# Optimization experiments

Hardware: AMD Instinct MI355X
Metric: run time of the kernel (lower is better)

## Reference

```python
import jax, jax.numpy as jnp
import numpy as np

EMBED_DIM = 768
NUM_HEADS = 12
HEAD_SIZE = EMBED_DIM // NUM_HEADS


def setup_inputs() -> dict:
    key = jax.random.key(0)
    ks = jax.random.split(key, 9)
    B, S, D = 4, 2048, EMBED_DIM
    scale = 1.0 / np.sqrt(D)
    x = jax.random.normal(ks[0], (B, S, D), dtype=jnp.float32)
    # Linear params (torch nn.Linear: y = x @ W.T + b); store W as [in, out] for einsum
    Wq = jax.random.normal(ks[1], (D, D), dtype=jnp.float32) * scale
    bq = jnp.zeros((D,), dtype=jnp.float32)
    Wk = jax.random.normal(ks[2], (D, D), dtype=jnp.float32) * scale
    bk = jnp.zeros((D,), dtype=jnp.float32)
    Wv = jax.random.normal(ks[3], (D, D), dtype=jnp.float32) * scale
    bv = jnp.zeros((D,), dtype=jnp.float32)
    Wo = jax.random.normal(ks[4], (D, D), dtype=jnp.float32) * scale
    bo = jnp.zeros((D,), dtype=jnp.float32)
    return {"x": x, "Wq": Wq, "bq": bq, "Wk": Wk, "bk": bk,
            "Wv": Wv, "bv": bv, "Wo": Wo, "bo": bo}


def reference(x, Wq, bq, Wk, bk, Wv, bv, Wo, bo):
    B, S, D = x.shape
    H, hs = NUM_HEADS, HEAD_SIZE
    scale = hs ** (-0.5)
    # Projections
    Q = (x @ Wq + bq).reshape(B, S, H, hs)
    K = (x @ Wk + bk).reshape(B, S, H, hs)
    V = (x @ Wv + bv).reshape(B, S, H, hs)
    # Batched attention over all heads (equivalent to the per-head loop:
    # torch view splits last dim into H contiguous chunks; concat of per-head
    # outputs along -1 restores the same layout)
    scores = jnp.einsum('bqhd,bkhd->bhqk', Q, K) * scale  # [B,H,S,S]
    attn = jax.nn.softmax(scores, axis=-1)
    out = jnp.einsum('bhqk,bkhd->bqhd', attn, V).reshape(B, S, D)
    # Output projection; dropout is identity in eval mode
    return out @ Wo + bo
```

## Files before the change

### kernel.cpp

```cpp
#include <hip/hip_runtime.h>

typedef unsigned short ushort_t;
typedef __bf16 bf16x8 __attribute__((ext_vector_type(8)));
typedef float floatx4 __attribute__((ext_vector_type(4)));

__device__ inline ushort_t f2bf(float f) {
    __bf16 h = (__bf16)f;
    return __builtin_bit_cast(ushort_t, h);
}

__device__ inline void gload16(const void* g, void* l) {
    __builtin_amdgcn_global_load_lds((const __attribute__((address_space(1))) void*)g,
                                     (__attribute__((address_space(3))) void*)l, 16, 0, 0);
}

__global__ __launch_bounds__(256) void prep_kernel(
    const float* __restrict__ x, ushort_t* __restrict__ xbf,
    const float* __restrict__ W0, const float* __restrict__ W1,
    const float* __restrict__ W2, const float* __restrict__ W3,
    ushort_t* __restrict__ T0, ushort_t* __restrict__ T1,
    ushort_t* __restrict__ T2, ushort_t* __restrict__ T3) {
    int bx = blockIdx.x;
    int tid = threadIdx.x;
    if (bx < 2304) {
        __shared__ float t[32][33];
        int w = bx / 576, rem = bx % 576;
        const float* W; ushort_t* T;
        switch (w) {
            case 0: W = W0; T = T0; break;
            case 1: W = W1; T = T1; break;
            case 2: W = W2; T = T2; break;
            default: W = W3; T = T3; break;
        }
        int n0 = (rem / 24) * 32, k0 = (rem % 24) * 32;
        int tx = tid & 31, ty = tid >> 5;
        for (int i = 0; i < 4; ++i)
            t[ty + i * 8][tx] = W[(k0 + ty + i * 8) * 768 + n0 + tx];
        __syncthreads();
        for (int i = 0; i < 4; ++i)
            T[(n0 + ty + i * 8) * 768 + k0 + tx] = f2bf(t[tx][ty + i * 8]);
    } else {
        int i = ((bx - 2304) * 256 + tid) * 4;
        float4 v = *(const float4*)(x + i);
        ushort4 u;
        u.x = f2bf(v.x); u.y = f2bf(v.y); u.z = f2bf(v.z); u.w = f2bf(v.w);
        *(ushort4*)(xbf + i) = u;
    }
}

__global__ __launch_bounds__(256) void gemm_qkv(
    const ushort_t* __restrict__ A,
    const ushort_t* __restrict__ Tq, const ushort_t* __restrict__ Tk, const ushort_t* __restrict__ Tv,
    const float* __restrict__ bq, const float* __restrict__ bk, const float* __restrict__ bv,
    ushort_t* __restrict__ Qb, ushort_t* __restrict__ Kb, ushort_t* __restrict__ Vtb) {
    __shared__ ushort_t sh[128 * 64 + 64 * 64];
    ushort_t* As = sh;
    ushort_t* Bs = sh + 128 * 64;
    int tid = threadIdx.x;
    int m0 = blockIdx.x * 128;
    int by = blockIdx.y;
    int which = by / 12;
    int n0 = (by % 12) * 64;
    const ushort_t* Bt = which == 0 ? Tq : (which == 1 ? Tk : Tv);
    const float* bias = which == 0 ? bq : (which == 1 ? bk : bv);

    int wave = tid >> 6;
    int lane = tid & 63;
    int ln = tid & 15;
    int quad = (tid >> 4) & 3;
    int wm = wave * 32;
    int lr = lane >> 3;
    int lc = (lane & 7) * 8;

    floatx4 acc[2][4];
    floatx4 z = {0.f, 0.f, 0.f, 0.f};
    for (int i = 0; i < 2; ++i)
        for (int j = 0; j < 4; ++j) acc[i][j] = z;

    for (int kt = 0; kt < 12; ++kt) {
        int k0 = kt * 64;
        __syncthreads();
        for (int i = 0; i < 4; ++i) {
            int c = wave * 4 + i;
            gload16(&A[(m0 + c * 8 + lr) * 768 + k0 + lc], &As[c * 512]);
        }
        for (int i = 0; i < 2; ++i) {
            int c = wave * 2 + i;
            gload16(&Bt[(n0 + c * 8 + lr) * 768 + k0 + lc], &Bs[c * 512]);
        }
        __syncthreads();
        for (int ks = 0; ks < 2; ++ks) {
            bf16x8 a[2], b[4];
            for (int i = 0; i < 2; ++i)
                a[i] = *(const bf16x8*)&As[(wm + i * 16 + ln) * 64 + ks * 32 + quad * 8];
            for (int j = 0; j < 4; ++j)
                b[j] = *(const bf16x8*)&Bs[(j * 16 + ln) * 64 + ks * 32 + quad * 8];
            for (int i = 0; i < 2; ++i)
                for (int j = 0; j < 4; ++j)
                    acc[i][j] = __builtin_amdgcn_mfma_f32_16x16x32_bf16(a[i], b[j], acc[i][j], 0, 0, 0);
        }
    }

    const float QSCALE = 0.125f * 1.44269504088896f;
    if (which != 2) {
        for (int i = 0; i < 2; ++i) {
            for (int j = 0; j < 4; ++j) {
                int gn = n0 + j * 16 + ln;
                float bia = bias[gn];
                int h = gn >> 6, dd = gn & 63;
                for (int r = 0; r < 4; ++r) {
                    int gm = m0 + wm + i * 16 + quad * 4 + r;
                    int bb = gm >> 11, ss = gm & 2047;
                    float v = acc[i][j][r] + bia;
                    if (which == 0) {
                        Qb[((bb * 12 + h) * 2048 + ss) * 64 + dd] = f2bf(v * QSCALE);
                    } else {
                        Kb[((bb * 12 + h) * 2048 + ss) * 64 + dd] = f2bf(v);
                    }
                }
            }
        }
    } else {
        __syncthreads();
        ushort_t* tr = sh;
        for (int j = 0; j < 4; ++j) {
            int nl = j * 16 + ln;
            float bia = bias[n0 + nl];
            for (int i = 0; i < 2; ++i) {
                ushort4 u;
                u.x = f2bf(acc[i][j][0] + bia);
                u.y = f2bf(acc[i][j][1] + bia);
                u.z = f2bf(acc[i][j][2] + bia);
                u.w = f2bf(acc[i][j][3] + bia);
                *(ushort4*)&tr[nl * 136 + wm + i * 16 + quad * 4] = u;
            }
        }
        __syncthreads();
        int bb = m0 >> 11, ss0 = m0 & 2047;
        int head = by % 12;
        for (int p = 0; p < 4; ++p) {
            int n = p * 16 + (tid >> 4);
            int mc = (tid & 15) * 8;
            uint4 v = *(const uint4*)&tr[n * 136 + mc];
            *(uint4*)&Vtb[(size_t)((bb * 12 + head) * 64 + n) * 2048 + ss0 + mc] = v;
        }
    }
}

__global__ __launch_bounds__(256, 2) void attn_kernel(
    const ushort_t* __restrict__ Qb, const ushort_t* __restrict__ Kb,
    const ushort_t* __restrict__ Vtb, ushort_t* __restrict__ Ob) {
    __shared__ ushort_t shm[4 * 64 * 72];
    const int PANEL = 64 * 72;
    int tid = threadIdx.x;
    int bid = blockIdx.x;
    int swz = (bid & 7) * 96 + (bid >> 3);
    int bh = swz >> 4;
    int qt = swz & 15;
    int wave = tid >> 6;
    int qh = wave >> 1;
    int kh = wave & 1;
    int ln = tid & 15;
    int quad = (tid >> 4) & 3;
    int q0 = qt * 128 + qh * 64;

    const ushort_t* Qp = Qb + (size_t)bh * 2048 * 64;
    const ushort_t* Kp = Kb + (size_t)bh * 2048 * 64;
    const ushort_t* Vp = Vtb + (size_t)bh * 64 * 2048;

    bf16x8 bqf[4][2];
    for (int g = 0; g < 4; ++g)
        for (int ks = 0; ks < 2; ++ks)
            bqf[g][ks] = *(const bf16x8*)&Qp[(q0 + g * 16 + ln) * 64 + ks * 32 + quad * 8];

    int srow = tid >> 3;
    int c8 = tid & 7;
    int scol = c8 * 8;
    int u = c8 & 3;
    int vcol = (c8 >> 2) * 32 + (u & 1) * 16 + (u >> 1) * 4;

    uint4 kreg[2], vreg[2];

    for (int p = 0; p < 2; ++p) {
        kreg[p] = *(const uint4*)&Kp[(p * 32 + srow) * 64 + scol];
        vreg[p] = *(const uint4*)&Vp[(p * 32 + srow) * 2048 + scol];
    }
    for (int p = 0; p < 2; ++p) {
        *(uint4*)&shm[(p * 32 + srow) * 72 + scol] = kreg[p];
        ushort_t* vb = &shm[2 * PANEL + (p * 32 + srow) * 72 + vcol];
        *(uint2*)vb = make_uint2(vreg[p].x, vreg[p].y);
        *(uint2*)(vb + 8) = make_uint2(vreg[p].z, vreg[p].w);
    }
    __syncthreads();

    floatx4 o_acc[4][4];
    float lsum[4] = {0.f, 0.f, 0.f, 0.f};
    floatx4 z = {0.f, 0.f, 0.f, 0.f};
    for (int g = 0; g < 4; ++g)
        for (int m4 = 0; m4 < 4; ++m4) o_acc[g][m4] = z;

    for (int kt = 0; kt < 32; ++kt) {
        int cur = kt & 1;
        if (kt < 31) {
            for (int p = 0; p < 2; ++p) {
                kreg[p] = *(const uint4*)&Kp[((kt + 1) * 64 + p * 32 + srow) * 64 + scol];
                vreg[p] = *(const uint4*)&Vp[(p * 32 + srow) * 2048 + (kt + 1) * 64 + scol];
            }
        }

        const ushort_t* KsH = shm + cur * PANEL;
        const ushort_t* VsH = shm + (2 + cur) * PANEL;

        bf16x8 ak[2][2];
        for (int m = 0; m < 2; ++m)
            for (int ks = 0; ks < 2; ++ks)
                ak[m][ks] = *(const bf16x8*)&KsH[((kh * 2 + m) * 16 + ln) * 72 + ks * 32 + quad * 8];

        floatx4 st[4][2];
        for (int g = 0; g < 4; ++g)
            for (int m = 0; m < 2; ++m) {
                floatx4 s = z;
                s = __builtin_amdgcn_mfma_f32_16x16x32_bf16(ak[m][0], bqf[g][0], s, 0, 0, 0);
                s = __builtin_amdgcn_mfma_f32_16x16x32_bf16(ak[m][1], bqf[g][1], s, 0, 0, 0);
                st[g][m] = s;
            }

        for (int g = 0; g < 4; ++g)
            for (int m = 0; m < 2; ++m)
                for (int r = 0; r < 4; ++r) {
                    float e = __builtin_amdgcn_exp2f(st[g][m][r]);
                    st[g][m][r] = e;
                    lsum[g] += e;
                }

        bf16x8 av[4];
        for (int m4 = 0; m4 < 4; ++m4)
            av[m4] = *(const bf16x8*)&VsH[(m4 * 16 + ln) * 72 + kh * 32 + quad * 8];

        for (int g = 0; g < 4; ++g) {
            bf16x8 b;
            b[0] = (__bf16)st[g][0][0];
            b[1] = (__bf16)st[g][0][1];
            b[2] = (__bf16)st[g][0][2];
            b[3] = (__bf16)st[g][0][3];
            b[4] = (__bf16)st[g][1][0];
            b[5] = (__bf16)st[g][1][1];
            b[6] = (__bf16)st[g][1][2];
            b[7] = (__bf16)st[g][1][3];
            for (int m4 = 0; m4 < 4; ++m4)
                o_acc[g][m4] = __builtin_amdgcn_mfma_f32_16x16x32_bf16(av[m4], b, o_acc[g][m4], 0, 0, 0);
        }

        if (kt < 31) {
            int nxt = cur ^ 1;
            ushort_t* Kn = shm + nxt * PANEL;
            ushort_t* Vn = shm + (2 + nxt) * PANEL;
            for (int p = 0; p < 2; ++p) {
                *(uint4*)&Kn[(p * 32 + srow) * 72 + scol] = kreg[p];
                ushort_t* vb = &Vn[(p * 32 + srow) * 72 + vcol];
                *(uint2*)vb = make_uint2(vreg[p].x, vreg[p].y);
                *(uint2*)(vb + 8) = make_uint2(vreg[p].z, vreg[p].w);
            }
        }
        __syncthreads();
    }

    for (int g = 0; g < 4; ++g) {
        lsum[g] += __shfl_xor(lsum[g], 16);
        lsum[g] += __shfl_xor(lsum[g], 32);
    }

    float* mbuf = (float*)shm;
    float* lbuf = mbuf + 2 * 64 * 68;
    if (kh == 1) {
        float* base = mbuf + qh * 64 * 68;
        for (int g = 0; g < 4; ++g) {
            for (int m4 = 0; m4 < 4; ++m4)
                *(floatx4*)&base[(g * 16 + ln) * 68 + m4 * 16 + quad * 4] = o_acc[g][m4];
            if (quad == 0) lbuf[qh * 64 + g * 16 + ln] = lsum[g];
        }
    }
    __syncthreads();

    int b = bh / 12, h = bh % 12;
    if (kh == 0) {
        float* base = mbuf + qh * 64 * 68;
        for (int g = 0; g < 4; ++g) {
            float inv = 1.f / (lsum[g] + lbuf[qh * 64 + g * 16 + ln]);
            int token = b * 2048 + q0 + g * 16 + ln;
            for (int m4 = 0; m4 < 4; ++m4) {
                floatx4 o2 = *(const floatx4*)&base[(g * 16 + ln) * 68 + m4 * 16 + quad * 4];
                for (int r = 0; r < 4; ++r)
                    Ob[token * 768 + h * 64 + m4 * 16 + quad * 4 + r] =
                        f2bf((o_acc[g][m4][r] + o2[r]) * inv);
            }
        }
    }
}

__global__ __launch_bounds__(256) void gemm_out(
    const ushort_t* __restrict__ A, const ushort_t* __restrict__ Bt,
    const float* __restrict__ bias, float* __restrict__ out) {
    __shared__ ushort_t As[128 * 64];
    __shared__ ushort_t Bs[64 * 64];
    int tid = threadIdx.x;
    int m0 = blockIdx.x * 128;
    int n0 = blockIdx.y * 64;

    int wave = tid >> 6;
    int lane = tid & 63;
    int ln = tid & 15;
    int quad = (tid >> 4) & 3;
    int wm = wave * 32;
    int lr = lane >> 3;
    int lc = (lane & 7) * 8;

    floatx4 acc[2][4];
    floatx4 z = {0.f, 0.f, 0.f, 0.f};
    for (int i = 0; i < 2; ++i)
        for (int j = 0; j < 4; ++j) acc[i][j] = z;

    for (int kt = 0; kt < 12; ++kt) {
        int k0 = kt * 64;
        __syncthreads();
        for (int i = 0; i < 4; ++i) {
            int c = wave * 4 + i;
            gload16(&A[(m0 + c * 8 + lr) * 768 + k0 + lc], &As[c * 512]);
        }
        for (int i = 0; i < 2; ++i) {
            int c = wave * 2 + i;
            gload16(&Bt[(n0 + c * 8 + lr) * 768 + k0 + lc], &Bs[c * 512]);
        }
        __syncthreads();
        for (int ks = 0; ks < 2; ++ks) {
            bf16x8 a[2], b[4];
            for (int i = 0; i < 2; ++i)
                a[i] = *(const bf16x8*)&As[(wm + i * 16 + ln) * 64 + ks * 32 + quad * 8];
            for (int j = 0; j < 4; ++j)
                b[j] = *(const bf16x8*)&Bs[(j * 16 + ln) * 64 + ks * 32 + quad * 8];
            for (int i = 0; i < 2; ++i)
                for (int j = 0; j < 4; ++j)
                    acc[i][j] = __builtin_amdgcn_mfma_f32_16x16x32_bf16(a[i], b[j], acc[i][j], 0, 0, 0);
        }
    }

    for (int i = 0; i < 2; ++i) {
        for (int j = 0; j < 4; ++j) {
            int gn = n0 + j * 16 + ln;
            float bia = bias[gn];
            for (int r = 0; r < 4; ++r) {
                int gm = m0 + wm + i * 16 + quad * 4 + r;
                out[gm * 768 + gn] = acc[i][j][r] + bia;
            }
        }
    }
}

extern "C" void kernel_launch(void* const* d_in, const int* in_sizes, int n_in,
                              void* d_out, int out_size, void* d_ws, size_t ws_size,
                              hipStream_t stream) {
    const float* x  = (const float*)d_in[0];
    const float* Wq = (const float*)d_in[1];
    const float* bq = (const float*)d_in[2];
    const float* Wk = (const float*)d_in[3];
    const float* bk = (const float*)d_in[4];
    const float* Wv = (const float*)d_in[5];
    const float* bv = (const float*)d_in[6];
    const float* Wo = (const float*)d_in[7];
    const float* bo = (const float*)d_in[8];

    const int NTOK = 4 * 2048;
    const int NELT = NTOK * 768;
    const int WELT = 768 * 768;

    ushort_t* xbf = (ushort_t*)d_ws;
    ushort_t* Tq  = xbf + NELT;
    ushort_t* Tk  = Tq + WELT;
    ushort_t* Tv  = Tk + WELT;
    ushort_t* To  = Tv + WELT;
    ushort_t* Qb  = To + WELT;
    ushort_t* Kb  = Qb + NELT;
    ushort_t* Vtb = Kb + NELT;
    ushort_t* Ob  = Vtb + NELT;

    prep_kernel<<<8448, 256, 0, stream>>>(x, xbf, Wq, Wk, Wv, Wo, Tq, Tk, Tv, To);
    gemm_qkv<<<dim3(64, 36), 256, 0, stream>>>(xbf, Tq, Tk, Tv, bq, bk, bv, Qb, Kb, Vtb);
    attn_kernel<<<768, 256, 0, stream>>>(Qb, Kb, Vtb, Ob);
    gemm_out<<<dim3(64, 12), 256, 0, stream>>>(Ob, To, bo, (float*)d_out);
}
```

Baseline: 214.4 us.

## Fuse Q, K, V projections into one block sharing the A tile

```diff
diff --git a/kernel.cpp b/kernel.cpp
--- a/kernel.cpp
+++ b/kernel.cpp
@@ -48,21 +48,16 @@
     }
 }
 
-__global__ __launch_bounds__(256) void gemm_qkv(
+__global__ __launch_bounds__(256, 2) void gemm_qkv(
     const ushort_t* __restrict__ A,
     const ushort_t* __restrict__ Tq, const ushort_t* __restrict__ Tk, const ushort_t* __restrict__ Tv,
     const float* __restrict__ bq, const float* __restrict__ bk, const float* __restrict__ bv,
     ushort_t* __restrict__ Qb, ushort_t* __restrict__ Kb, ushort_t* __restrict__ Vtb) {
-    __shared__ ushort_t sh[128 * 64 + 64 * 64];
-    ushort_t* As = sh;
-    ushort_t* Bs = sh + 128 * 64;
+    __shared__ ushort_t sh[128 * 64 + 3 * 64 * 64];
     int tid = threadIdx.x;
     int m0 = blockIdx.x * 128;
     int by = blockIdx.y;
-    int which = by / 12;
-    int n0 = (by % 12) * 64;
-    const ushort_t* Bt = which == 0 ? Tq : (which == 1 ? Tk : Tv);
-    const float* bias = which == 0 ? bq : (which == 1 ? bk : bv);
+    int n0 = by * 64;
 
     int wave = tid >> 6;
     int lane = tid & 63;
@@ -72,37 +67,48 @@
     int lr = lane >> 3;
     int lc = (lane & 7) * 8;
 
-    floatx4 acc[2][4];
+    floatx4 acc[3][2][4];
     floatx4 z = {0.f, 0.f, 0.f, 0.f};
-    for (int i = 0; i < 2; ++i)
-        for (int j = 0; j < 4; ++j) acc[i][j] = z;
+    for (int w = 0; w < 3; ++w)
+        for (int i = 0; i < 2; ++i)
+            for (int j = 0; j < 4; ++j) acc[w][i][j] = z;
 
     for (int kt = 0; kt < 12; ++kt) {
         int k0 = kt * 64;
         __syncthreads();
         for (int i = 0; i < 4; ++i) {
             int c = wave * 4 + i;
-            gload16(&A[(m0 + c * 8 + lr) * 768 + k0 + lc], &As[c * 512]);
+            gload16(&A[(m0 + c * 8 + lr) * 768 + k0 + lc], &sh[c * 512]);
         }
         for (int i = 0; i < 2; ++i) {
             int c = wave * 2 + i;
-            gload16(&Bt[(n0 + c * 8 + lr) * 768 + k0 + lc], &Bs[c * 512]);
+            int goff = (n0 + c * 8 + lr) * 768 + k0 + lc;
+            gload16(&Tq[goff], &sh[8192 + c * 512]);
+            gload16(&Tk[goff], &sh[12288 + c * 512]);
+            gload16(&Tv[goff], &sh[16384 + c * 512]);
         }
         __syncthreads();
         for (int ks = 0; ks < 2; ++ks) {
-            bf16x8 a[2], b[4];
+            bf16x8 a[2];
             for (int i = 0; i < 2; ++i)
-                a[i] = *(const bf16x8*)&As[(wm + i * 16 + ln) * 64 + ks * 32 + quad * 8];
-            for (int j = 0; j < 4; ++j)
-                b[j] = *(const bf16x8*)&Bs[(j * 16 + ln) * 64 + ks * 32 + quad * 8];
-            for (int i = 0; i < 2; ++i)
+                a[i] = *(const bf16x8*)&sh[(wm + i * 16 + ln) * 64 + ks * 32 + quad * 8];
+            for (int w = 0; w < 3; ++w) {
+                const ushort_t* Bs = &sh[8192 + w * 4096];
+                bf16x8 b[4];
                 for (int j = 0; j < 4; ++j)
-                    acc[i][j] = __builtin_amdgcn_mfma_f32_16x16x32_bf16(a[i], b[j], acc[i][j], 0, 0, 0);
+                    b[j] = *(const bf16x8*)&Bs[(j * 16 + ln) * 64 + ks * 32 + quad * 8];
+                for (int i = 0; i < 2; ++i)
+                    for (int j = 0; j < 4; ++j)
+                        acc[w][i][j] = __builtin_amdgcn_mfma_f32_16x16x32_bf16(a[i], b[j], acc[w][i][j], 0, 0, 0);
+            }
         }
     }
 
     const float QSCALE = 0.125f * 1.44269504088896f;
-    if (which != 2) {
+    for (int w = 0; w < 2; ++w) {
+        const float* bias = w == 0 ? bq : bk;
+        ushort_t* QK = w == 0 ? Qb : Kb;
+        float scale = w == 0 ? QSCALE : 1.0f;
         for (int i = 0; i < 2; ++i) {
             for (int j = 0; j < 4; ++j) {
                 int gn = n0 + j * 16 + ln;
@@ -111,33 +117,29 @@
                 for (int r = 0; r < 4; ++r) {
                     int gm = m0 + wm + i * 16 + quad * 4 + r;
                     int bb = gm >> 11, ss = gm & 2047;
-                    float v = acc[i][j][r] + bia;
-                    if (which == 0) {
-                        Qb[((bb * 12 + h) * 2048 + ss) * 64 + dd] = f2bf(v * QSCALE);
-                    } else {
-                        Kb[((bb * 12 + h) * 2048 + ss) * 64 + dd] = f2bf(v);
-                    }
+                    QK[((bb * 12 + h) * 2048 + ss) * 64 + dd] = f2bf((acc[w][i][j][r] + bia) * scale);
                 }
             }
         }
-    } else {
-        __syncthreads();
+    }
+    __syncthreads();
+    {
         ushort_t* tr = sh;
         for (int j = 0; j < 4; ++j) {
             int nl = j * 16 + ln;
-            float bia = bias[n0 + nl];
+            float bia = bv[n0 + nl];
             for (int i = 0; i < 2; ++i) {
                 ushort4 u;
-                u.x = f2bf(acc[i][j][0] + bia);
-                u.y = f2bf(acc[i][j][1] + bia);
-                u.z = f2bf(acc[i][j][2] + bia);
-                u.w = f2bf(acc[i][j][3] + bia);
+                u.x = f2bf(acc[2][i][j][0] + bia);
+                u.y = f2bf(acc[2][i][j][1] + bia);
+                u.z = f2bf(acc[2][i][j][2] + bia);
+                u.w = f2bf(acc[2][i][j][3] + bia);
                 *(ushort4*)&tr[nl * 136 + wm + i * 16 + quad * 4] = u;
             }
         }
         __syncthreads();
         int bb = m0 >> 11, ss0 = m0 & 2047;
-        int head = by % 12;
+        int head = by;
         for (int p = 0; p < 4; ++p) {
             int n = p * 16 + (tid >> 4);
             int mc = (tid & 15) * 8;
@@ -384,7 +386,7 @@
     ushort_t* Ob  = Vtb + NELT;
 
     prep_kernel<<<8448, 256, 0, stream>>>(x, xbf, Wq, Wk, Wv, Wo, Tq, Tk, Tv, To);
-    gemm_qkv<<<dim3(64, 36), 256, 0, stream>>>(xbf, Tq, Tk, Tv, bq, bk, bv, Qb, Kb, Vtb);
+    gemm_qkv<<<dim3(64, 12), 256, 0, stream>>>(xbf, Tq, Tk, Tv, bq, bk, bv, Qb, Kb, Vtb);
     attn_kernel<<<768, 256, 0, stream>>>(Qb, Kb, Vtb, Ob);
     gemm_out<<<dim3(64, 12), 256, 0, stream>>>(Ob, To, bo, (float*)d_out);
 }
```

Result: faster. 205.5 us (median of 2 runs) (-4.1%).
